# Performance work log

Hardware: AMD Instinct MI355X
Metric: run time of the kernel (lower is better)

The kernel has to match this reference:

```python
import jax, jax.numpy as jnp
import numpy as np
import math

B, T, D, CAP = 4, 1024, 512, 32768
MEM_UPDATE_MOMENTUM = 0.99
MEM_NEW_DATA_RATE = 0.01

def setup_inputs() -> dict:
    key = jax.random.key(0)
    k1, k2, k3, k4, k5 = jax.random.split(key, 5)
    keys = jax.random.normal(k1, (B, T, D), dtype=jnp.float32)
    values = jax.random.normal(k2, (B, T, D), dtype=jnp.float32)
    importance = jax.random.uniform(k3, (B, T, 1), dtype=jnp.float32)
    query = jax.random.normal(k4, (B, T, D), dtype=jnp.float32)
    # xavier_uniform on (1, CAP, D): fan_in=D, fan_out=CAP (torch treats dim-1/dim-2)
    bound = math.sqrt(6.0 / (CAP + D))
    mem = jax.random.uniform(k5, (1, CAP, D), minval=-bound, maxval=bound, dtype=jnp.float32)
    return {"keys": keys, "values": values, "importance": importance, "query": query, "mem": mem}

def reference(keys, values, importance, query, mem):
    b, t, d = keys.shape
    cap = mem.shape[1]
    # ---- write ----
    scores = jnp.einsum('btd,ocd->btc', keys, mem)          # [b, t, cap]
    usage = jax.nn.softmax(scores, axis=-1).sum(axis=1)     # [b, cap]
    combined = importance.mean(axis=(1, 2))                 # [b]
    write_priority = combined[:, None] + 0.1 * usage        # [b, cap]
    k = min(t, cap)
    _, indices = jax.lax.top_k(write_priority, k)           # [b, k]
    values_write = values[:, :k]                            # [b, k, d]
    scatter = jnp.zeros((b, cap, d), dtype=keys.dtype)
    scatter = scatter.at[jnp.arange(b)[:, None], indices].set(values_write)
    new_mem = mem * MEM_UPDATE_MOMENTUM + scatter.mean(axis=0, keepdims=True) * MEM_NEW_DATA_RATE
    # ---- read (against updated memory) ----
    attn = jnp.einsum('bqd,ocd->bqc', query, new_mem) / math.sqrt(d)
    attn = jax.nn.softmax(attn, axis=-1)                    # [b, q, cap]
    out = jnp.einsum('bqc,ocd->bqd', attn, new_mem)         # [b, q, d]
    return out
```

## Files before the change

### kernel.cpp

```cpp
#include <hip/hip_runtime.h>
#include <hip/hip_fp8.h>

typedef float f32x4 __attribute__((ext_vector_type(4)));
typedef short s16x8 __attribute__((ext_vector_type(8)));
typedef short s16x4 __attribute__((ext_vector_type(4)));
typedef unsigned short ush;
typedef unsigned char u8;

constexpr int Bn = 4, Tn = 1024, Dn = 512, CAPn = 32768, Kn = 1024;
constexpr int ROWS = Bn * Tn;
constexpr float SCALE = 0.044194173824159216f;
constexpr float SC64 = SCALE / 64.0f;
constexpr float MOM = 0.99f;
constexpr float RATE_B = 0.0025f;

constexpr size_t OFF_NM8   = 0;
constexpr size_t OFF_NMT   = 33554432;
constexpr size_t OFF_OPART = 67108864;
constexpr size_t OFF_KHF   = 67108864;
constexpr size_t OFF_ZPART = 75497472;
constexpr size_t OFF_PRIO  = 83886080;
constexpr size_t OFF_RANK  = 84410368;
constexpr size_t OFF_COMB  = 84934656;
constexpr size_t OFF_ZP2   = 100663296;

#define MFMA(a, b, c) __builtin_amdgcn_mfma_f32_16x16x32_bf16((a), (b), (c), 0, 0, 0)
#define MFMAH(a, b, c) __builtin_amdgcn_mfma_f32_16x16x32_f16((a), (b), (c), 0, 0, 0)
#define MFMA8(a, b, c) __builtin_amdgcn_mfma_f32_16x16x32_fp8_fp8((a), (b), (c), 0, 0, 0)

__device__ __forceinline__ ush bfrn(float x) {
  unsigned u = __float_as_uint(x);
  return (ush)((u + 0x7FFFu + ((u >> 16) & 1u)) >> 16);
}
__device__ __forceinline__ float bff(ush h) { return __uint_as_float(((unsigned)h) << 16); }
__device__ __forceinline__ ush f16rn(float x) {
  _Float16 h = (_Float16)x;
  return *(ush*)&h;
}
__device__ __forceinline__ u8 f8rn(float x) {
  __hip_fp8_e4m3 v(x);
  return (u8)v.__x;
}

__device__ __forceinline__ void gl16(const void* g, void* l) {
  __builtin_amdgcn_global_load_lds(
      (const __attribute__((address_space(1))) void*)(uintptr_t)g,
      (__attribute__((address_space(3))) void*)(uintptr_t)l, 16, 0, 0);
}

__global__ void k_combined(const float* __restrict__ imp, float* __restrict__ comb) {
  __shared__ float red[256];
  int b = blockIdx.x;
  float s = 0.f;
  for (int t = threadIdx.x; t < Tn; t += 256) s += imp[(size_t)b * Tn + t];
  red[threadIdx.x] = s;
  __syncthreads();
  for (int off = 128; off > 0; off >>= 1) {
    if (threadIdx.x < (unsigned)off) red[threadIdx.x] += red[threadIdx.x + off];
    __syncthreads();
  }
  if (threadIdx.x == 0) comb[b] = red[0] * (1.0f / Tn);
}

__global__ void k_cvt_f16(const float* __restrict__ x, ush* __restrict__ o) {
  size_t i = ((size_t)blockIdx.x * 256 + threadIdx.x) * 4;
  f32x4 v = *(const f32x4*)&x[i];
  s16x4 h;
#pragma unroll
  for (int j = 0; j < 4; ++j) h[j] = (short)f16rn(v[j]);
  *(s16x4*)&o[i] = h;
}

__global__ __launch_bounds__(256, 2) void k_rowexp(const ush* __restrict__ Ahf,
                                                   const ush* __restrict__ Bhf,
                                                   float* __restrict__ zpart) {
  __shared__ ush Bs[64 * 512];
  __shared__ float red[2][64];
  const int tid = threadIdx.x;
  const int lane = tid & 63, wid = tid >> 6;
  const int wc2 = wid >> 1, wt = wid & 1;
  const int l15 = lane & 15, g = lane >> 4;
  const int cb = blockIdx.x;
  const int cBase = cb * 64;

  s16x8 afr[2][16];
#pragma unroll
  for (int mi = 0; mi < 2; ++mi) {
    int c = cBase + wc2 * 32 + mi * 16 + l15;
#pragma unroll
    for (int ks = 0; ks < 16; ++ks)
      afr[mi][ks] = *(const s16x8*)&Ahf[(size_t)c * Dn + ks * 32 + g * 8];
  }

  for (int tt = 0; tt < 64; ++tt) {
    const int tBase = tt * 64;
#pragma unroll
    for (int rr = 0; rr < 16; ++rr) {
      int idx = rr * 256 + tid;
      int row = idx >> 6, ch = idx & 63;
      gl16(&Bhf[(size_t)(tBase + row) * Dn + ((ch ^ (row & 7)) << 3)],
           &Bs[rr * 2048 + wid * 512]);
    }
    __syncthreads();
    f32x4 S[2][2];
#pragma unroll
    for (int mi = 0; mi < 2; ++mi)
#pragma unroll
      for (int ni = 0; ni < 2; ++ni) S[mi][ni] = (f32x4){0.f, 0.f, 0.f, 0.f};
#pragma unroll
    for (int ks = 0; ks < 16; ++ks) {
      s16x8 bfr[2];
#pragma unroll
      for (int ni = 0; ni < 2; ++ni) {
        int trow = wt * 32 + ni * 16 + l15;
        bfr[ni] = *(const s16x8*)&Bs[trow * 512 + (((ks * 4 + g) ^ (trow & 7)) * 8)];
      }
#pragma unroll
      for (int mi = 0; mi < 2; ++mi)
#pragma unroll
        for (int ni = 0; ni < 2; ++ni) S[mi][ni] = MFMAH(afr[mi][ks], bfr[ni], S[mi][ni]);
    }
    float tacc[2] = {0.f, 0.f};
#pragma unroll
    for (int mi = 0; mi < 2; ++mi)
#pragma unroll
      for (int ni = 0; ni < 2; ++ni)
#pragma unroll
        for (int r = 0; r < 4; ++r) tacc[ni] += __expf(S[mi][ni][r]);
#pragma unroll
    for (int ni = 0; ni < 2; ++ni) {
      float v = tacc[ni];
      v += __shfl_xor(v, 16);
      v += __shfl_xor(v, 32);
      tacc[ni] = v;
    }
    if (g == 0) {
      red[wc2][wt * 32 + l15] = tacc[0];
      red[wc2][wt * 32 + 16 + l15] = tacc[1];
    }
    __syncthreads();
    if (tid < 64) zpart[(size_t)cb * ROWS + tBase + tid] = red[0][tid] + red[1][tid];
  }
}

__global__ void k_invl(const float* __restrict__ zpart, float* __restrict__ invl) {
  int t = blockIdx.x * 256 + threadIdx.x;
  float s = 0.f;
  for (int cb = 0; cb < 512; ++cb) s += zpart[(size_t)cb * ROWS + t];
  invl[t] = 1.0f / s;
}

__global__ __launch_bounds__(256, 3) void k_usage(const ush* __restrict__ mhf,
                                                  const ush* __restrict__ khf,
                                                  const float* __restrict__ invl,
                                                  const float* __restrict__ comb,
                                                  float* __restrict__ prio) {
  __shared__ ush Ah[128 * 64], Bh[128 * 64];
  const int tid = threadIdx.x;
  const int lane = tid & 63, w = tid >> 6;
  const int l15 = lane & 15, g = lane >> 4;
  const int cBase = blockIdx.x * 128;
  const int b = blockIdx.y;
  const ush* khb = khf + (size_t)b * Tn * Dn;
  const int r0 = tid >> 3, u0 = tid & 7;
  const int usw = (u0 ^ (r0 & 7)) << 3;

  float uacc[2][4] = {{0.f, 0.f, 0.f, 0.f}, {0.f, 0.f, 0.f, 0.f}};
  for (int tt = 0; tt < 8; ++tt) {
    f32x4 S[2][8];
#pragma unroll
    for (int mi = 0; mi < 2; ++mi)
#pragma unroll
      for (int ni = 0; ni < 8; ++ni) S[mi][ni] = (f32x4){0.f, 0.f, 0.f, 0.f};
    for (int kk = 0; kk < 8; ++kk) {
      __syncthreads();
      {
        size_t a0 = (size_t)(cBase + r0) * Dn + kk * 64 + usw;
        size_t a1 = (size_t)(cBase + r0 + 64) * Dn + kk * 64 + usw;
        gl16(&mhf[a0], &Ah[w * 512]);
        gl16(&mhf[a1], &Ah[4096 + w * 512]);
        size_t b0 = (size_t)(tt * 128 + r0) * Dn + kk * 64 + usw;
        size_t b1 = (size_t)(tt * 128 + r0 + 64) * Dn + kk * 64 + usw;
        gl16(&khb[b0], &Bh[w * 512]);
        gl16(&khb[b1], &Bh[4096 + w * 512]);
      }
      __syncthreads();
#pragma unroll
      for (int ks2 = 0; ks2 < 2; ++ks2) {
        s16x8 ah[2];
#pragma unroll
        for (int mi = 0; mi < 2; ++mi) {
          int crow = w * 32 + mi * 16 + l15;
          ah[mi] = *(const s16x8*)&Ah[crow * 64 + (((ks2 * 4 + g) ^ (crow & 7)) * 8)];
        }
#pragma unroll
        for (int ni = 0; ni < 8; ++ni) {
          int trow = ni * 16 + l15;
          s16x8 bh = *(const s16x8*)&Bh[trow * 64 + (((ks2 * 4 + g) ^ (trow & 7)) * 8)];
#pragma unroll
          for (int mi = 0; mi < 2; ++mi) S[mi][ni] = MFMAH(ah[mi], bh, S[mi][ni]);
        }
      }
    }
#pragma unroll
    for (int ni = 0; ni < 8; ++ni) {
      float il = invl[b * Tn + tt * 128 + ni * 16 + l15];
#pragma unroll
      for (int mi = 0; mi < 2; ++mi)
#pragma unroll
        for (int r = 0; r < 4; ++r) uacc[mi][r] += __expf(S[mi][ni][r]) * il;
    }
  }
#pragma unroll
  for (int mi = 0; mi < 2; ++mi)
#pragma unroll
    for (int r = 0; r < 4; ++r) {
      float v = uacc[mi][r];
      v += __shfl_xor(v, 1);
      v += __shfl_xor(v, 2);
      v += __shfl_xor(v, 4);
      v += __shfl_xor(v, 8);
      if (l15 == 0)
        prio[(size_t)b * CAPn + cBase + w * 32 + mi * 16 + g * 4 + r] =
            comb[b] + 0.1f * v;
    }
}

__global__ void k_rankinit(int* __restrict__ rank) {
  rank[blockIdx.x * 256 + threadIdx.x] = Kn;
}

__global__ __launch_bounds__(1024) void k_select(const float* __restrict__ prio,
                                                 int* __restrict__ rank) {
  const int b = blockIdx.x;
  const float* p = prio + (size_t)b * CAPn;
  __shared__ int hist[256];
  __shared__ unsigned long long s_pref;
  __shared__ int s_krem;
  __shared__ int s_cnt;
  __shared__ unsigned long long selk[Kn];
  const int tid = threadIdx.x;
  if (tid == 0) { s_pref = 0ull; s_krem = Kn; s_cnt = 0; }

#define KEYOF(c, kk)                                                         \
  {                                                                          \
    unsigned mb_ = __float_as_uint(p[(c)]);                                  \
    mb_ = (mb_ & 0x80000000u) ? ~mb_ : (mb_ | 0x80000000u);                  \
    (kk) = ((unsigned long long)mb_ << 32) | (unsigned)(0xFFFFFFFFu - (c));  \
  }

  __syncthreads();
  for (int pos = 56; pos >= 0; pos -= 8) {
    if (tid < 256) hist[tid] = 0;
    __syncthreads();
    unsigned long long pref = s_pref;
    unsigned long long maskhi = (pos == 56) ? 0ull : (~0ull << (pos + 8));
    for (int c = tid; c < CAPn; c += 1024) {
      unsigned long long k;
      KEYOF(c, k);
      if ((k & maskhi) == pref) atomicAdd(&hist[(int)((k >> pos) & 255)], 1);
    }
    __syncthreads();
    if (tid == 0) {
      int krem = s_krem;
      int d = 255;
      for (;; --d) {
        int h = hist[d];
        if (krem <= h || d == 0) break;
        krem -= h;
      }
      s_pref = pref | ((unsigned long long)d << pos);
      s_krem = krem;
    }
    __syncthreads();
  }
  unsigned long long T = s_pref;
  for (int c = tid; c < CAPn; c += 1024) {
    unsigned long long k;
    KEYOF(c, k);
    if (k >= T) {
      int idx = atomicAdd(&s_cnt, 1);
      selk[idx] = k;
    }
  }
  __syncthreads();
  unsigned long long mine = selk[tid];
  int r = 0;
  for (int j = 0; j < Kn; ++j) r += (selk[j] > mine) ? 1 : 0;
  int c = (int)(0xFFFFFFFFu - (unsigned)(mine & 0xFFFFFFFFull));
  rank[(size_t)b * CAPn + c] = r;
#undef KEYOF
}

__global__ void k_newmem8(const float* __restrict__ mem, const float* __restrict__ values,
                          const int* __restrict__ rank, u8* __restrict__ nm8) {
  int gid = blockIdx.x * 256 + threadIdx.x;
  int c = gid >> 7;
  int q = (gid & 127) << 2;
  f32x4 m = *(const f32x4*)&mem[(size_t)c * Dn + q];
  f32x4 acc = {0.f, 0.f, 0.f, 0.f};
#pragma unroll
  for (int b = 0; b < Bn; ++b) {
    int r = rank[(size_t)b * CAPn + c];
    if (r < Kn) acc += *(const f32x4*)&values[((size_t)b * Tn + r) * Dn + q];
  }
  f32x4 res = (m * MOM + acc * RATE_B) * 64.0f;
  union { u8 b[4]; unsigned w; } out;
#pragma unroll
  for (int j = 0; j < 4; ++j) out.b[j] = f8rn(res[j]);
  *(unsigned*)&nm8[(size_t)c * Dn + q] = out.w;
}

__global__ __launch_bounds__(256) void k_nmT(const float* __restrict__ mem,
                                             const float* __restrict__ values,
                                             const int* __restrict__ rank,
                                             ush* __restrict__ nmT) {
  __shared__ ush tile[64][65];
  int cBase = blockIdx.x * 64, dBase = blockIdx.y * 64;
  int tid = threadIdx.x;
  int c = tid >> 2, dq = (tid & 3) * 16;
  int rr[4];
#pragma unroll
  for (int b = 0; b < Bn; ++b) rr[b] = rank[(size_t)b * CAPn + cBase + c];
#pragma unroll
  for (int j = 0; j < 4; ++j) {
    f32x4 m = *(const f32x4*)&mem[(size_t)(cBase + c) * Dn + dBase + dq + j * 4];
    f32x4 a = {0.f, 0.f, 0.f, 0.f};
#pragma unroll
    for (int b = 0; b < Bn; ++b)
      if (rr[b] < Kn)
        a += *(const f32x4*)&values[((size_t)b * Tn + rr[b]) * Dn + dBase + dq + j * 4];
    f32x4 res = m * MOM + a * RATE_B;
#pragma unroll
    for (int jj = 0; jj < 4; ++jj) tile[c][dq + j * 4 + jj] = bfrn(res[jj]);
  }
  __syncthreads();
  int drow = tid >> 2, cq = (tid & 3) * 16;
#pragma unroll
  for (int k = 0; k < 2; ++k) {
    s16x8 v;
#pragma unroll
    for (int j = 0; j < 8; ++j) v[j] = (short)tile[cq + k * 8 + j][drow];
    *(s16x8*)&nmT[(size_t)(dBase + drow) * CAPn + cBase + cq + k * 8] = v;
  }
}

#define WAITV2 asm volatile("s_waitcnt vmcnt(2)" ::: "memory")
#define WAITL0 asm volatile("s_waitcnt lgkmcnt(0)" ::: "memory")
#define BAR __builtin_amdgcn_s_barrier()
__global__ __launch_bounds__(512, 1) void k_attnout(
    const float* __restrict__ query, const u8* __restrict__ nm8,
    const ush* __restrict__ nmT, ush* __restrict__ opart,
    float* __restrict__ zp2) {
  __shared__ __align__(16) u8 L[131072];
  __shared__ float zred[128];
  __shared__ float zacc[128];
  constexpr int LMS = 0, LMT = 49152, LPS = 98304;
  const int tid = threadIdx.x;
  const int lane = tid & 63, w = tid >> 6;
  const int l15 = lane & 15, g = lane >> 4;
  const int cy = blockIdx.x;
  const int qBase = blockIdx.y * 128;
  const int q = w * 16 + l15;
  const int r0 = tid >> 3, u0 = tid & 7;
  const int usw = (u0 ^ (r0 & 7)) << 3;
  const int usw8 = (u0 ^ (r0 & 7)) << 4;

  auto stage_ms = [&](int buf, int cb_, int kk) {
    const u8* src = nm8 + (size_t)cb_ * Dn + kk * 128;
    gl16(&src[(size_t)r0 * Dn + usw8], &L[LMS + buf * 16384 + w * 1024]);
    gl16(&src[(size_t)(r0 + 64) * Dn + usw8], &L[LMS + buf * 16384 + 8192 + w * 1024]);
  };
  auto stage_mt = [&](int buf, int cb_, int u) {
    const ush* src = nmT + (size_t)((u >> 1) * 128) * CAPn + cb_ + (u & 1) * 64;
    gl16(&src[(size_t)r0 * CAPn + usw], &L[LMT + buf * 16384 + w * 1024]);
    gl16(&src[(size_t)(r0 + 64) * CAPn + usw], &L[LMT + buf * 16384 + 8192 + w * 1024]);
  };

  long qfr8[16];
  {
    const float* qsrc = query + (size_t)(qBase + q) * Dn;
#pragma unroll
    for (int ks = 0; ks < 16; ++ks) {
      f32x4 a = *(const f32x4*)&qsrc[ks * 32 + g * 8];
      f32x4 b = *(const f32x4*)&qsrc[ks * 32 + g * 8 + 4];
      union { u8 c[8]; long l; } u;
#pragma unroll
      for (int j = 0; j < 4; ++j) {
        u.c[j] = f8rn(a[j]);
        u.c[4 + j] = f8rn(b[j]);
      }
      qfr8[ks] = u.l;
    }
  }

  f32x4 O[32];
#pragma unroll
  for (int i = 0; i < 32; ++i) O[i] = (f32x4){0.f, 0.f, 0.f, 0.f};
  if (tid < 128) zacc[tid] = 0.f;

  stage_ms(0, cy * 4096, 0);
  stage_ms(1, cy * 4096, 1);

  for (int ct = 0; ct < 32; ++ct) {
    const int cBase = cy * 4096 + ct * 128;
    const int cNext = cy * 4096 + ((ct + 1) & 31) * 128;

    f32x4 S[8];
#pragma unroll
    for (int i = 0; i < 8; ++i) S[i] = (f32x4){0.f, 0.f, 0.f, 0.f};
#pragma unroll
    for (int kk = 0; kk < 4; ++kk) {
      WAITV2;
      WAITL0;
      BAR;
      if (kk < 2) stage_ms((kk + 2) % 3, cBase, kk + 2);
      else if (kk == 2) stage_mt(0, cBase, 0);
      else stage_mt(1, cBase, 1);
      __builtin_amdgcn_s_setprio(1);
#pragma unroll
      for (int ks = 0; ks < 4; ++ks) {
#pragma unroll
        for (int mi = 0; mi < 8; ++mi) {
          int row = mi * 16 + l15;
          long a = *(const long*)&L[LMS + (kk % 3) * 16384 + row * 128 +
                                    (((ks * 2 + (g >> 1)) ^ (row & 7)) << 4) +
                                    (g & 1) * 8];
          S[mi] = MFMA8(a, qfr8[kk * 4 + ks], S[mi]);
        }
      }
      __builtin_amdgcn_s_setprio(0);
    }

    float zl = 0.f;
#pragma unroll
    for (int mi = 0; mi < 8; ++mi) {
      s16x4 p;
#pragma unroll
      for (int r = 0; r < 4; ++r) {
        float e = __expf(S[mi][r] * SC64);
        zl += e;
        p[r] = (short)bfrn(e);
      }
      int u16 = (mi * 2 + (g >> 1)) ^ l15;
      *(s16x4*)&L[LPS + q * 256 + u16 * 16 + (g & 1) * 8] = p;
    }
    zl += __shfl_xor(zl, 16);
    zl += __shfl_xor(zl, 32);
    if (g == 0) zred[q] = zl;
    WAITL0;
    BAR;
    if (tid < 128) zacc[tid] += zred[tid];

#pragma unroll
    for (int u = 0; u < 8; ++u) {
      WAITV2;
      WAITL0;
      BAR;
      if (u < 6) stage_mt((u + 2) % 3, cBase, u + 2);
      else if (u == 6) stage_ms(0, cNext, 0);
      else stage_ms(1, cNext, 1);
      __builtin_amdgcn_s_setprio(1);
      const int hh = u & 1;
#pragma unroll
      for (int kc = 0; kc < 2; ++kc) {
        int u16 = (hh * 8 + kc * 4 + g) ^ l15;
        s16x8 pb = *(const s16x8*)&L[LPS + q * 256 + u16 * 16];
#pragma unroll
        for (int mi = 0; mi < 8; ++mi) {
          int row = mi * 16 + l15;
          s16x8 am = *(const s16x8*)&L[LMT + (u % 3) * 16384 + row * 128 +
                                       (((kc * 4 + g) ^ (row & 7)) << 4)];
          O[(u >> 1) * 8 + mi] = MFMA(am, pb, O[(u >> 1) * 8 + mi]);
        }
      }
      __builtin_amdgcn_s_setprio(0);
    }
  }

  __syncthreads();
  if (tid < 128) zp2[(size_t)cy * ROWS + qBase + tid] = zacc[tid];
#pragma unroll
  for (int ds = 0; ds < 4; ++ds) {
    __syncthreads();
#pragma unroll
    for (int mi = 0; mi < 8; ++mi) {
      s16x4 ov;
#pragma unroll
      for (int r = 0; r < 4; ++r) ov[r] = (short)bfrn(O[ds * 8 + mi][r]);
      int u16 = (mi * 2 + (g >> 1)) ^ l15;
      *(s16x4*)&L[LPS + q * 256 + u16 * 16 + (g & 1) * 8] = ov;
    }
    __syncthreads();
#pragma unroll
    for (int i = 0; i < 4; ++i) {
      int slot = i * 512 + tid;
      int qq = slot >> 4, u16 = slot & 15;
      s16x8 v = *(const s16x8*)&L[LPS + qq * 256 + ((u16 ^ (qq & 15)) << 4)];
      *(s16x8*)&opart[((size_t)cy * ROWS + qBase + qq) * Dn + ds * 128 + u16 * 8] = v;
    }
  }
}

__global__ void k_merge(const ush* __restrict__ opart, const float* __restrict__ zp2,
                        float* __restrict__ out) {
  size_t i = ((size_t)blockIdx.x * 256 + threadIdx.x) * 4;
  int row = (int)(i >> 9);
  float z = 0.f;
#pragma unroll
  for (int cyy = 0; cyy < 8; ++cyy) z += zp2[(size_t)cyy * ROWS + row];
  float inv = 1.0f / z;
  f32x4 acc = {0.f, 0.f, 0.f, 0.f};
#pragma unroll
  for (int cyy = 0; cyy < 8; ++cyy) {
    s16x4 a = *(const s16x4*)&opart[(size_t)cyy * ROWS * Dn + i];
#pragma unroll
    for (int j = 0; j < 4; ++j) acc[j] += bff((ush)a[j]);
  }
#pragma unroll
  for (int j = 0; j < 4; ++j) acc[j] *= inv;
  *(f32x4*)&out[i] = acc;
}

extern "C" void kernel_launch(void* const* d_in, const int* in_sizes, int n_in,
                              void* d_out, int out_size, void* d_ws, size_t ws_size,
                              hipStream_t stream) {
  const float* keys = (const float*)d_in[0];
  const float* values = (const float*)d_in[1];
  const float* importance = (const float*)d_in[2];
  const float* query = (const float*)d_in[3];
  const float* mem = (const float*)d_in[4];
  char* wsb = (char*)d_ws;
  u8* nm8    = (u8*)(wsb + OFF_NM8);
  ush* nmT   = (ush*)(wsb + OFF_NMT);
  ush* mhf   = (ush*)(wsb + OFF_NMT);
  ush* khf   = (ush*)(wsb + OFF_KHF);
  ush* opart = (ush*)(wsb + OFF_OPART);
  float* zpart = (float*)(wsb + OFF_ZPART);
  float* prio  = (float*)(wsb + OFF_PRIO);
  int* rank    = (int*)(wsb + OFF_RANK);
  float* comb  = (float*)(wsb + OFF_COMB);
  float* zp2   = (float*)(wsb + OFF_ZP2);
  float* invl1 = (float*)(wsb + OFF_COMB + 64);
  float* out = (float*)d_out;

  k_combined<<<Bn, 256, 0, stream>>>(importance, comb);
  k_cvt_f16<<<(ROWS * Dn / 4) / 256, 256, 0, stream>>>(keys, khf);
  k_cvt_f16<<<(CAPn * Dn / 4) / 256, 256, 0, stream>>>(mem, mhf);
  k_rowexp<<<CAPn / 64, 256, 0, stream>>>(mhf, khf, zpart);
  k_invl<<<ROWS / 256, 256, 0, stream>>>(zpart, invl1);
  k_usage<<<dim3(CAPn / 128, Bn), 256, 0, stream>>>(mhf, khf, invl1, comb, prio);
  k_rankinit<<<(Bn * CAPn) / 256, 256, 0, stream>>>(rank);
  k_select<<<Bn, 1024, 0, stream>>>(prio, rank);
  k_newmem8<<<(CAPn * Dn / 4) / 256, 256, 0, stream>>>(mem, values, rank, nm8);
  k_nmT<<<dim3(CAPn / 64, Dn / 64), 256, 0, stream>>>(mem, values, rank, nmT);
  k_attnout<<<dim3(8, ROWS / 128), 512, 0, stream>>>(query, nm8, nmT, opart, zp2);
  k_merge<<<(ROWS * Dn / 4) / 256, 256, 0, stream>>>(opart, zp2, out);
}
```

Baseline: 857.4 us.

## Use 32x32x16 bf16 MFMA for P·V accumulation in attention-output kernel

```diff
diff --git a/kernel.cpp b/kernel.cpp
--- a/kernel.cpp
+++ b/kernel.cpp
@@ -2,6 +2,7 @@
 #include <hip/hip_fp8.h>
 
 typedef float f32x4 __attribute__((ext_vector_type(4)));
+typedef float f32x16 __attribute__((ext_vector_type(16)));
 typedef short s16x8 __attribute__((ext_vector_type(8)));
 typedef short s16x4 __attribute__((ext_vector_type(4)));
 typedef unsigned short ush;
@@ -27,6 +28,7 @@
 #define MFMA(a, b, c) __builtin_amdgcn_mfma_f32_16x16x32_bf16((a), (b), (c), 0, 0, 0)
 #define MFMAH(a, b, c) __builtin_amdgcn_mfma_f32_16x16x32_f16((a), (b), (c), 0, 0, 0)
 #define MFMA8(a, b, c) __builtin_amdgcn_mfma_f32_16x16x32_fp8_fp8((a), (b), (c), 0, 0, 0)
+#define MFMAB32(a, b, c) __builtin_amdgcn_mfma_f32_32x32x16_bf16((a), (b), (c), 0, 0, 0)
 
 __device__ __forceinline__ ush bfrn(float x) {
   unsigned u = __float_as_uint(x);
@@ -359,6 +361,8 @@
   const int tid = threadIdx.x;
   const int lane = tid & 63, w = tid >> 6;
   const int l15 = lane & 15, g = lane >> 4;
+  const int l31 = lane & 31, h = lane >> 5;
+  const int dt = w & 3, qg = w >> 2;
   const int cy = blockIdx.x;
   const int qBase = blockIdx.y * 128;
   const int q = w * 16 + l15;
@@ -394,9 +398,9 @@
     }
   }
 
-  f32x4 O[32];
-#pragma unroll
-  for (int i = 0; i < 32; ++i) O[i] = (f32x4){0.f, 0.f, 0.f, 0.f};
+  f32x16 O[8];
+#pragma unroll
+  for (int i = 0; i < 8; ++i) O[i] = (f32x16)(0.f);
   if (tid < 128) zacc[tid] = 0.f;
 
   stage_ms(0, cy * 4096, 0);
@@ -461,17 +465,17 @@
       else if (u == 6) stage_ms(0, cNext, 0);
       else stage_ms(1, cNext, 1);
       __builtin_amdgcn_s_setprio(1);
-      const int hh = u & 1;
-#pragma unroll
-      for (int kc = 0; kc < 2; ++kc) {
-        int u16 = (hh * 8 + kc * 4 + g) ^ l15;
-        s16x8 pb = *(const s16x8*)&L[LPS + q * 256 + u16 * 16];
-#pragma unroll
-        for (int mi = 0; mi < 8; ++mi) {
-          int row = mi * 16 + l15;
-          s16x8 am = *(const s16x8*)&L[LMT + (u % 3) * 16384 + row * 128 +
-                                       (((kc * 4 + g) ^ (row & 7)) << 4)];
-          O[(u >> 1) * 8 + mi] = MFMA(am, pb, O[(u >> 1) * 8 + mi]);
+#pragma unroll
+      for (int kc = 0; kc < 4; ++kc) {
+        int d = dt * 32 + l31;
+        s16x8 am = *(const s16x8*)&L[LMT + (u % 3) * 16384 + d * 128 +
+                                     (((kc * 2 + h) ^ (d & 7)) << 4)];
+#pragma unroll
+        for (int tqi = 0; tqi < 2; ++tqi) {
+          int qq = qg * 64 + tqi * 32 + l31;
+          s16x8 pb = *(const s16x8*)&L[LPS + qq * 256 +
+                                       ((((u & 1) * 8 + kc * 2 + h) ^ (qq & 15)) << 4)];
+          O[(u >> 1) * 2 + tqi] = MFMAB32(am, pb, O[(u >> 1) * 2 + tqi]);
         }
       }
       __builtin_amdgcn_s_setprio(0);
@@ -481,23 +485,29 @@
   __syncthreads();
   if (tid < 128) zp2[(size_t)cy * ROWS + qBase + tid] = zacc[tid];
 #pragma unroll
-  for (int ds = 0; ds < 4; ++ds) {
-    __syncthreads();
-#pragma unroll
-    for (int mi = 0; mi < 8; ++mi) {
-      s16x4 ov;
-#pragma unroll
-      for (int r = 0; r < 4; ++r) ov[r] = (short)bfrn(O[ds * 8 + mi][r]);
-      int u16 = (mi * 2 + (g >> 1)) ^ l15;
-      *(s16x4*)&L[LPS + q * 256 + u16 * 16 + (g & 1) * 8] = ov;
+  for (int p = 0; p < 4; ++p) {
+    __syncthreads();
+    if (qg == (p >> 1)) {
+      const int tqi = p & 1;
+#pragma unroll
+      for (int db = 0; db < 4; ++db)
+#pragma unroll
+        for (int r2 = 0; r2 < 4; ++r2) {
+          s16x4 ov;
+#pragma unroll
+          for (int j = 0; j < 4; ++j) ov[j] = (short)bfrn(O[db * 2 + tqi][r2 * 4 + j]);
+          int u8i = db * 32 + dt * 8 + r2 * 2 + h;
+          int u8s = u8i ^ ((l31 & 15) << 1);
+          *(s16x4*)&L[LPS + l31 * 1024 + u8s * 8] = ov;
+        }
     }
     __syncthreads();
 #pragma unroll
     for (int i = 0; i < 4; ++i) {
       int slot = i * 512 + tid;
-      int qq = slot >> 4, u16 = slot & 15;
-      s16x8 v = *(const s16x8*)&L[LPS + qq * 256 + ((u16 ^ (qq & 15)) << 4)];
-      *(s16x8*)&opart[((size_t)cy * ROWS + qBase + qq) * Dn + ds * 128 + u16 * 8] = v;
+      int ql = slot >> 6, u16 = slot & 63;
+      s16x8 v = *(const s16x8*)&L[LPS + ql * 1024 + ((u16 ^ (ql & 15)) << 4)];
+      *(s16x8*)&opart[((size_t)cy * ROWS + qBase + p * 32 + ql) * Dn + u16 * 8] = v;
     }
   }
 }
```

Result: no change. 855.4 us (-0.2%).
